# Kernel tuning notes

Measured on AMD Instinct MI355X. Metric: run time of the kernel, lower is better.

## Reference

```python
import jax, jax.numpy as jnp
import numpy as np

B, L, D, Z = 256, 120, 192, 512
H = 2 * Z  # LSTM hidden size


def _lstm_cell(x, h, c, Wih, Whh, bih, bhh):
    # torch LSTMCell gate order: i, f, g, o
    gates = x @ Wih.T + h @ Whh.T + bih + bhh
    i, f, g, o = jnp.split(gates, 4, axis=-1)
    c = jax.nn.sigmoid(f) * c + jax.nn.sigmoid(i) * jnp.tanh(g)
    h = jax.nn.sigmoid(o) * jnp.tanh(c)
    return h, c


def setup_inputs() -> dict:
    key = jax.random.key(0)
    ks = iter(jax.random.split(key, 64))
    def nrm(*shape):
        return jax.random.normal(next(ks), shape, jnp.float32) * 0.02
    inp = {}
    inp["x"] = jax.random.normal(next(ks), (B, L, D), jnp.float32)
    inp["x_lengths"] = jax.random.randint(next(ks), (B,), 1, L + 1)
    # encoder params
    inp["ln_w"] = jnp.ones((L, D), jnp.float32)
    inp["ln_b"] = jnp.zeros((L, D), jnp.float32)
    inp["enc_w"], inp["enc_b"] = nrm(Z, D), nrm(Z)
    for d in ("f", "b"):
        inp["Wih_" + d] = nrm(4 * H, Z)
        inp["Whh_" + d] = nrm(4 * H, H)
        inp["bih_" + d] = nrm(4 * H)
        inp["bhh_" + d] = nrm(4 * H)
    inp["mu1_w"], inp["mu1_b"] = nrm(H, 2 * H), nrm(H)
    inp["mu2_w"], inp["mu2_b"] = nrm(Z, H), nrm(Z)
    inp["lv1_w"], inp["lv1_b"] = nrm(H, 2 * H), nrm(H)
    inp["lv2_w"], inp["lv2_b"] = nrm(Z, H), nrm(Z)
    # decoder params
    inp["dz_w"], inp["dz_b"] = nrm(Z, Z), nrm(Z)
    inp["p1_w"], inp["p1_b"] = nrm(Z, Z), nrm(Z)
    inp["p2_w"], inp["p2_b"] = nrm(D, Z), nrm(D)
    inp["dWih"] = nrm(4 * H, Z + D)
    inp["dWhh"] = nrm(4 * H, H)
    inp["dbih"] = nrm(4 * H)
    inp["dbhh"] = nrm(4 * H)
    inp["l1_w"], inp["l1_b"] = nrm(Z, H), nrm(Z)
    inp["l2_w"], inp["l2_b"] = nrm(D, Z), nrm(D)
    return inp


def _forward(x, x_lengths, ln_w, ln_b, enc_w, enc_b,
             Wih_f, Whh_f, bih_f, bhh_f, Wih_b, Whh_b, bih_b, bhh_b,
             mu1_w, mu1_b, mu2_w, mu2_b, lv1_w, lv1_b, lv2_w, lv2_b,
             dz_w, dz_b, p1_w, p1_b, p2_w, p2_b,
             dWih, dWhh, dbih, dbhh, l1_w, l1_b, l2_w, l2_b):
    relu = jax.nn.relu
    # LayerNorm with normalized_shape=[L, D]: normalize jointly over last two dims
    m = x.mean(axis=(1, 2), keepdims=True)
    v = x.var(axis=(1, 2), keepdims=True)
    xn = (x - m) / jnp.sqrt(v + 1e-5) * ln_w + ln_b
    xe = relu(xn @ enc_w.T + enc_b)          # [B, L, Z]
    xs = xe.transpose(1, 0, 2)               # [L, B, Z]
    ts = jnp.arange(L)

    def make_step(Wih, Whh, bih, bhh):
        def step(carry, inp_t):
            h, c = carry
            xt, t = inp_t
            nh, nc = _lstm_cell(xt, h, c, Wih, Whh, bih, bhh)
            act = (t < x_lengths)[:, None]   # packed-sequence mask
            h = jnp.where(act, nh, h)
            c = jnp.where(act, nc, c)
            return (h, c), jnp.where(act, h, 0.0)  # padded outputs are zero
        return step

    h0 = jnp.zeros((B, H), x.dtype)
    _, out_f = jax.lax.scan(make_step(Wih_f, Whh_f, bih_f, bhh_f), (h0, h0), (xs, ts))
    # backward direction: scan reversed; carry stays zero until first valid step
    _, out_b = jax.lax.scan(make_step(Wih_b, Whh_b, bih_b, bhh_b), (h0, h0), (xs, ts), reverse=True)
    out = jnp.concatenate([out_f, out_b], axis=-1)          # [L, B, 2H]
    pooled = out.sum(axis=0) / x_lengths[:, None].astype(x.dtype)
    mu = relu(pooled @ mu1_w.T + mu1_b) @ mu2_w.T + mu2_b
    log_var = relu(pooled @ lv1_w.T + lv1_b) @ lv2_w.T + lv2_b
    eps = jax.random.normal(jax.random.key(42), mu.shape, mu.dtype)
    z = eps * jnp.exp(0.5 * log_var) + mu
    # decoder with per-step feedback
    xz = relu(z @ dz_w.T + dz_b)
    pose0 = relu(xz @ p1_w.T + p1_b) @ p2_w.T + p2_b

    def dec_step(carry, _):
        h, c, pose = carry
        inp_t = jnp.concatenate([xz, pose], axis=1)
        h, c = _lstm_cell(inp_t, h, c, dWih, dWhh, dbih, dbhh)
        pose = relu(h @ l1_w.T + l1_b) @ l2_w.T + l2_b  # residual=False
        return (h, c, pose), pose

    _, dec = jax.lax.scan(dec_step, (h0, h0, pose0), None, length=L)
    return x, dec.transpose(1, 0, 2), x_lengths, mu, log_var, z


def reference(x, x_lengths, ln_w, ln_b, enc_w, enc_b,
              Wih_f, Whh_f, bih_f, bhh_f, Wih_b, Whh_b, bih_b, bhh_b,
              mu1_w, mu1_b, mu2_w, mu2_b, lv1_w, lv1_b, lv2_w, lv2_b,
              dz_w, dz_b, p1_w, p1_b, p2_w, p2_b,
              dWih, dWhh, dbih, dbhh, l1_w, l1_b, l2_w, l2_b):
    return _forward(x, x_lengths, ln_w, ln_b, enc_w, enc_b,
                    Wih_f, Whh_f, bih_f, bhh_f, Wih_b, Whh_b, bih_b, bhh_b,
                    mu1_w, mu1_b, mu2_w, mu2_b, lv1_w, lv1_b, lv2_w, lv2_b,
                    dz_w, dz_b, p1_w, p1_b, p2_w, p2_b,
                    dWih, dWhh, dbih, dbhh, l1_w, l1_b, l2_w, l2_b)
```

## Files before the change

### kernel.cpp

```cpp
#include <hip/hip_runtime.h>

typedef __bf16 bf16_t;
typedef __bf16 bf16x8 __attribute__((ext_vector_type(8)));
typedef __bf16 bf16x4 __attribute__((ext_vector_type(4)));
typedef float  f32x4  __attribute__((ext_vector_type(4)));

#define DEV __device__ __forceinline__

constexpr int Bn = 256;
constexpr int Ln = 120;
constexpr int Dn = 192;
constexpr int Zn = 512;
constexpr int Hn = 1024;
constexpr int KE = Zn + Hn;
constexpr int KD = Zn + Dn + Hn;
constexpr int CATD = Zn + Dn;
constexpr int NBLK = 256;

DEV f32x4 mfma16(bf16x8 a, bf16x8 b, f32x4 c) {
  return __builtin_amdgcn_mfma_f32_16x16x32_bf16(a, b, c, 0, 0, 0);
}
DEV bf16x8 ldb8(const bf16_t* p) { return *reinterpret_cast<const bf16x8*>(p); }
DEV float sigf(float x) { return 1.f / (1.f + expf(-x)); }
DEV unsigned short b2u(bf16_t v) { union { bf16_t b; unsigned short u; } x; x.b = v; return x.u; }

DEV void ld4i(const bf16_t* p0, const bf16_t* p1, const bf16_t* p2, const bf16_t* p3,
              bf16x8& o0, bf16x8& o1, bf16x8& o2, bf16x8& o3) {
  asm volatile(
      "global_load_dwordx4 %0, %4, off sc0 sc1\n\t"
      "global_load_dwordx4 %1, %5, off sc0 sc1\n\t"
      "global_load_dwordx4 %2, %6, off sc0 sc1\n\t"
      "global_load_dwordx4 %3, %7, off sc0 sc1"
      : "=&v"(o0), "=&v"(o1), "=&v"(o2), "=&v"(o3)
      : "v"(p0), "v"(p1), "v"(p2), "v"(p3)
      : "memory");
}
DEV void ld8i(const bf16_t* p0, const bf16_t* p1, const bf16_t* p2, const bf16_t* p3,
              const bf16_t* p4, const bf16_t* p5, const bf16_t* p6, const bf16_t* p7,
              bf16x8& o0, bf16x8& o1, bf16x8& o2, bf16x8& o3,
              bf16x8& o4, bf16x8& o5, bf16x8& o6, bf16x8& o7) {
  asm volatile(
      "global_load_dwordx4 %0, %8, off sc0 sc1\n\t"
      "global_load_dwordx4 %1, %9, off sc0 sc1\n\t"
      "global_load_dwordx4 %2, %10, off sc0 sc1\n\t"
      "global_load_dwordx4 %3, %11, off sc0 sc1\n\t"
      "global_load_dwordx4 %4, %12, off sc0 sc1\n\t"
      "global_load_dwordx4 %5, %13, off sc0 sc1\n\t"
      "global_load_dwordx4 %6, %14, off sc0 sc1\n\t"
      "global_load_dwordx4 %7, %15, off sc0 sc1"
      : "=&v"(o0), "=&v"(o1), "=&v"(o2), "=&v"(o3),
        "=&v"(o4), "=&v"(o5), "=&v"(o6), "=&v"(o7)
      : "v"(p0), "v"(p1), "v"(p2), "v"(p3), "v"(p4), "v"(p5), "v"(p6), "v"(p7)
      : "memory");
}
DEV void vwait0() {
  asm volatile("s_waitcnt vmcnt(0)" ::: "memory");
  __builtin_amdgcn_sched_barrier(0);
}

DEV void st16c(bf16_t* p, bf16x8 v) {
  asm volatile("global_store_dwordx4 %0, %1, off sc0 sc1" :: "v"(p), "v"(v) : "memory");
}
DEV void st8c(bf16_t* p, bf16x4 v) {
  asm volatile("global_store_dwordx2 %0, %1, off sc0 sc1" :: "v"(p), "v"(v) : "memory");
}
DEV void st2c(bf16_t* p, unsigned short v) {
  asm volatile("global_store_short %0, %1, off sc0 sc1" :: "v"(p), "v"(v) : "memory");
}

DEV void gbar(unsigned* bar, unsigned epoch, int bid) {
  asm volatile("s_waitcnt vmcnt(0)" ::: "memory");
  __syncthreads();
  if (threadIdx.x == 0) {
    int g = bid & 7;
    unsigned a = __hip_atomic_fetch_add(bar + g * 16, 1u, __ATOMIC_RELAXED,
                                        __HIP_MEMORY_SCOPE_AGENT);
    if (a == epoch * 32u - 1u) {
      unsigned b = __hip_atomic_fetch_add(bar + 128, 1u, __ATOMIC_RELAXED,
                                          __HIP_MEMORY_SCOPE_AGENT);
      if (b == epoch * 8u - 1u)
        __hip_atomic_store(bar + 192, epoch, __ATOMIC_RELAXED, __HIP_MEMORY_SCOPE_AGENT);
    }
    while (__hip_atomic_load(bar + 192, __ATOMIC_RELAXED, __HIP_MEMORY_SCOPE_AGENT) < epoch)
      __builtin_amdgcn_s_sleep(2);
  }
  __syncthreads();
}

__global__ void k_cast_all(
    const float* __restrict__ s0, const float* __restrict__ s1,
    const float* __restrict__ s2, const float* __restrict__ s3,
    const float* __restrict__ s4, const float* __restrict__ s5,
    const float* __restrict__ s6, const float* __restrict__ s7,
    const float* __restrict__ s8, const float* __restrict__ s9,
    bf16_t* __restrict__ d0, bf16_t* __restrict__ d1,
    bf16_t* __restrict__ d2, bf16_t* __restrict__ d3,
    bf16_t* __restrict__ d4, bf16_t* __restrict__ d5,
    bf16_t* __restrict__ d6, bf16_t* __restrict__ d7,
    bf16_t* __restrict__ d8, bf16_t* __restrict__ d9) {
  const long TOT = 1646592;
  for (long gidx = blockIdx.x * blockDim.x + threadIdx.x; gidx < TOT;
       gidx += (long)gridDim.x * blockDim.x) {
    const float* s; bf16_t* d; long r = gidx;
    if      (r < 24576)                      { s = s0; d = d0; }
    else if ((r -= 24576)   < 524288)        { s = s1; d = d1; }
    else if ((r -= 524288)  < 524288)        { s = s2; d = d2; }
    else if ((r -= 524288)  < 131072)        { s = s3; d = d3; }
    else if ((r -= 131072)  < 131072)        { s = s4; d = d4; }
    else if ((r -= 131072)  < 65536)         { s = s5; d = d5; }
    else if ((r -= 65536)   < 65536)         { s = s6; d = d6; }
    else if ((r -= 65536)   < 24576)         { s = s7; d = d7; }
    else if ((r -= 24576)   < 131072)        { s = s8; d = d8; }
    else    { r -= 131072;                     s = s9; d = d9; }
    float4 v = reinterpret_cast<const float4*>(s)[r];
    bf16x4 o;
    o[0] = (bf16_t)v.x; o[1] = (bf16_t)v.y; o[2] = (bf16_t)v.z; o[3] = (bf16_t)v.w;
    *reinterpret_cast<bf16x4*>(d + 4 * r) = o;
  }
}

__global__ void k_layernorm(const float* __restrict__ x, const float* __restrict__ w,
                            const float* __restrict__ bsh, float* __restrict__ out0,
                            bf16_t* __restrict__ xn) {
  const int n = Ln * Dn;
  int b = blockIdx.x;
  const float* xb = x + (long)b * n;
  float s = 0.f, s2 = 0.f;
  for (int i = threadIdx.x; i < n; i += 256) { float v = xb[i]; s += v; s2 += v * v; }
  for (int off = 32; off; off >>= 1) { s += __shfl_down(s, off); s2 += __shfl_down(s2, off); }
  __shared__ float sh[8];
  int wave = threadIdx.x >> 6, lane = threadIdx.x & 63;
  if (lane == 0) { sh[wave] = s; sh[4 + wave] = s2; }
  __syncthreads();
  if (threadIdx.x == 0) {
    float S = sh[0] + sh[1] + sh[2] + sh[3];
    float S2 = sh[4] + sh[5] + sh[6] + sh[7];
    float m = S / n;
    float var = fmaxf(S2 / n - m * m, 0.f);
    sh[0] = m; sh[1] = rsqrtf(var + 1e-5f);
  }
  __syncthreads();
  float m = sh[0], inv = sh[1];
  for (int i = threadIdx.x; i < n; i += 256) {
    float v = xb[i];
    out0[(long)b * n + i] = v;
    xn[(long)b * n + i] = (bf16_t)((v - m) * inv * w[i] + bsh[i]);
  }
}

template <int ACT, bool XSPERM>
__global__ __launch_bounds__(256) void k_gemm(
    const bf16_t* __restrict__ A, int lda,
    const bf16_t* __restrict__ W, int ldw,
    const float* __restrict__ bias,
    float* __restrict__ outF, long ldoF,
    bf16_t* __restrict__ outB, int ldoB,
    int K) {
  int lane = threadIdx.x & 63, wave = threadIdx.x >> 6;
  int l15 = lane & 15, q = lane >> 4;
  int m0 = blockIdx.x * 64 + (wave >> 1) * 32;
  int n0 = blockIdx.y * 64 + (wave & 1) * 32;
  f32x4 acc00 = {}, acc01 = {}, acc10 = {}, acc11 = {};
  const bf16_t* Ap = A + (long)(m0 + l15) * lda + q * 8;
  const bf16_t* Wp = W + (long)(n0 + l15) * ldw + q * 8;
  long a16 = (long)16 * lda, w16 = (long)16 * ldw;
  for (int k0 = 0; k0 < K; k0 += 32) {
    bf16x8 a0 = ldb8(Ap + k0);
    bf16x8 a1 = ldb8(Ap + a16 + k0);
    bf16x8 b0 = ldb8(Wp + k0);
    bf16x8 b1 = ldb8(Wp + w16 + k0);
    acc00 = mfma16(a0, b0, acc00);
    acc01 = mfma16(a0, b1, acc01);
    acc10 = mfma16(a1, b0, acc10);
    acc11 = mfma16(a1, b1, acc11);
  }
#pragma unroll
  for (int mi = 0; mi < 2; ++mi)
#pragma unroll
    for (int ni = 0; ni < 2; ++ni) {
      f32x4 acc = (mi == 0) ? (ni == 0 ? acc00 : acc01) : (ni == 0 ? acc10 : acc11);
#pragma unroll
      for (int r = 0; r < 4; ++r) {
        int m = m0 + mi * 16 + q * 4 + r;
        int nn = n0 + ni * 16 + l15;
        float v = acc[r] + bias[nn];
        if (ACT == 1) v = fmaxf(v, 0.f);
        if (outF) outF[(long)m * ldoF + nn] = v;
        if (outB) {
          long row = XSPERM ? ((long)(m % Ln) * Bn + m / Ln) : m;
          outB[row * (long)ldoB + nn] = (bf16_t)v;
        }
      }
    }
}

constexpr int ENC_CH = KE / 32;
constexpr int ENC_SMEM_W = 2 * ENC_CH * 64 * 16;
constexpr int ENC_SMEM_G = 4 * 64 * 33 * 4;
constexpr int ENC_SMEM = ENC_SMEM_W + ENC_SMEM_G + 128;

__global__ __launch_bounds__(256, 1) void k_enc_persist(
    const bf16_t* __restrict__ xs,
    const float* __restrict__ WihF, const float* __restrict__ WhhF,
    const float* __restrict__ bihF, const float* __restrict__ bhhF,
    const float* __restrict__ WihB, const float* __restrict__ WhhB,
    const float* __restrict__ bihB, const float* __restrict__ bhhB,
    const int* __restrict__ lens,
    bf16_t* __restrict__ hf0, bf16_t* __restrict__ hf1,
    bf16_t* __restrict__ hb0, bf16_t* __restrict__ hb1,
    bf16_t* __restrict__ pooledb, float* __restrict__ out_len,
    unsigned* bar) {
  extern __shared__ char smem[];
  bf16x8* Wl = (bf16x8*)smem;
  float* Gbuf = (float*)(smem + ENC_SMEM_W);
  float* bias_l = (float*)(smem + ENC_SMEM_W + ENC_SMEM_G);

  int bid = blockIdx.x;
  int dir = bid >> 7;
  int j0 = (bid & 127) * 8;
  const float* Wih = dir ? WihB : WihF;
  const float* Whh = dir ? WhhB : WhhF;
  const float* bih = dir ? bihB : bihF;
  const float* bhh = dir ? bhhB : bhhF;
  bf16_t* h0 = dir ? hb0 : hf0;
  bf16_t* h1 = dir ? hb1 : hf1;

  int tid = threadIdx.x;
  for (int f = tid; f < 2 * ENC_CH * 64; f += 256) {
    int ni = f / (ENC_CH * 64);
    int rem = f - ni * (ENC_CH * 64);
    int c = rem >> 6, sub = rem & 63;
    int sl = sub & 15, sq = sub >> 4;
    int r = ni * 16 + sl;
    int grow = (r >> 3) * Hn + j0 + (r & 7);
    int k = c * 32 + sq * 8;
    const float* src = (k < Zn) ? (Wih + (long)grow * Zn + k)
                                : (Whh + (long)grow * Hn + (k - Zn));
    bf16x8 v;
#pragma unroll
    for (int e = 0; e < 8; ++e) v[e] = (bf16_t)src[e];
    Wl[f] = v;
  }
  if (tid < 32) {
    int grow = (tid >> 3) * Hn + j0 + (tid & 7);
    bias_l[tid] = bih[grow] + bhh[grow];
  }
  if (bid == 0) out_len[tid] = (float)lens[tid];
  __syncthreads();

  int wave = tid >> 6, lane = tid & 63;
  int l15 = lane & 15, q = lane >> 4;
  int mrow = wave * 64 + l15;
  int m = wave * 64 + lane;
  int mylen = lens[m];
  float c_reg[8] = {}, h_reg[8] = {}, pool_reg[8] = {};
  float* Gw = Gbuf + wave * (64 * 33);
  const bf16x8* Wl0 = Wl;
  const bf16x8* Wl1 = Wl + ENC_CH * 64;
  const long h16 = (long)16 * Hn;

#define ENC_HISS(A, c) do { long hk_ = (long)(c) * 32 - Zn;                               \
    ld8i(hrow + hk_,            hrow + h16 + hk_,                                         \
         hrow + 2 * h16 + hk_,  hrow + 3 * h16 + hk_,                                     \
         hrow + hk_ + 32,       hrow + h16 + hk_ + 32,                                    \
         hrow + 2 * h16 + hk_ + 32, hrow + 3 * h16 + hk_ + 32,                            \
         A[0], A[1], A[2], A[3], A[4], A[5], A[6], A[7]); } while (0)
#define ENC_HCONS(A, c) do {                                                              \
    { bf16x8 b0 = Wl0[(c) * 64 + lane], b1 = Wl1[(c) * 64 + lane];                        \
      acc[0][0] = mfma16(A[0], b0, acc[0][0]); acc[0][1] = mfma16(A[0], b1, acc[0][1]);   \
      acc[1][0] = mfma16(A[1], b0, acc[1][0]); acc[1][1] = mfma16(A[1], b1, acc[1][1]);   \
      acc[2][0] = mfma16(A[2], b0, acc[2][0]); acc[2][1] = mfma16(A[2], b1, acc[2][1]);   \
      acc[3][0] = mfma16(A[3], b0, acc[3][0]); acc[3][1] = mfma16(A[3], b1, acc[3][1]); } \
    { bf16x8 b0 = Wl0[((c) + 1) * 64 + lane], b1 = Wl1[((c) + 1) * 64 + lane];            \
      acc[0][0] = mfma16(A[4], b0, acc[0][0]); acc[0][1] = mfma16(A[4], b1, acc[0][1]);   \
      acc[1][0] = mfma16(A[5], b0, acc[1][0]); acc[1][1] = mfma16(A[5], b1, acc[1][1]);   \
      acc[2][0] = mfma16(A[6], b0, acc[2][0]); acc[2][1] = mfma16(A[6], b1, acc[2][1]);   \
      acc[3][0] = mfma16(A[7], b0, acc[3][0]); acc[3][1] = mfma16(A[7], b1, acc[3][1]); } \
  } while (0)
#define ENC_STEP(Acur, Anext, c) vwait0(); ENC_HISS(Anext, (c) + 2); ENC_HCONS(Acur, c);

  for (int t = 0; t < Ln; ++t) {
    int tt = dir ? (Ln - 1 - t) : t;
    const bf16_t* xt = xs + (long)tt * Bn * Zn;
    const bf16_t* hprev = (t & 1) ? h1 : h0;
    bf16_t* hcur = (t & 1) ? h0 : h1;

    f32x4 acc[4][2] = {};
    const bf16_t* xrow = xt + (long)mrow * Zn + q * 8;
    const bf16_t* hrow = hprev + (long)mrow * Hn + q * 8;

    bf16x8 HA[8], HB[8];
    ENC_HISS(HA, 16);
    for (int c = 0; c < Zn / 32; ++c) {
      bf16x8 b0 = Wl0[c * 64 + lane];
      bf16x8 b1 = Wl1[c * 64 + lane];
#pragma unroll
      for (int mi = 0; mi < 4; ++mi) {
        bf16x8 a = ldb8(xrow + (long)mi * 16 * Zn + c * 32);
        acc[mi][0] = mfma16(a, b0, acc[mi][0]);
        acc[mi][1] = mfma16(a, b1, acc[mi][1]);
      }
    }
    ENC_STEP(HA, HB, 16) ENC_STEP(HB, HA, 18) ENC_STEP(HA, HB, 20) ENC_STEP(HB, HA, 22)
    ENC_STEP(HA, HB, 24) ENC_STEP(HB, HA, 26) ENC_STEP(HA, HB, 28) ENC_STEP(HB, HA, 30)
    ENC_STEP(HA, HB, 32) ENC_STEP(HB, HA, 34) ENC_STEP(HA, HB, 36) ENC_STEP(HB, HA, 38)
    ENC_STEP(HA, HB, 40) ENC_STEP(HB, HA, 42) ENC_STEP(HA, HB, 44)
    vwait0(); ENC_HCONS(HB, 46);

#pragma unroll
    for (int mi = 0; mi < 4; ++mi)
#pragma unroll
      for (int ni = 0; ni < 2; ++ni)
#pragma unroll
        for (int r = 0; r < 4; ++r)
          Gw[(mi * 16 + q * 4 + r) * 33 + ni * 16 + l15] = acc[mi][ni][r];
    __syncthreads();
    bool act = tt < mylen;
    const float* Gr = Gw + lane * 33;
    bf16x8 hpack;
#pragma unroll
    for (int jj = 0; jj < 8; ++jj) {
      float Gi = Gr[jj] + bias_l[jj];
      float Gf = Gr[8 + jj] + bias_l[8 + jj];
      float Gg = Gr[16 + jj] + bias_l[16 + jj];
      float Go = Gr[24 + jj] + bias_l[24 + jj];
      float cn = sigf(Gf) * c_reg[jj] + sigf(Gi) * tanhf(Gg);
      float hn = sigf(Go) * tanhf(cn);
      if (act) { c_reg[jj] = cn; h_reg[jj] = hn; pool_reg[jj] += hn; }
      hpack[jj] = (bf16_t)h_reg[jj];
    }
    st16c(hcur + (long)m * Hn + j0, hpack);
    if (t != Ln - 1) gbar(bar, (unsigned)(t + 1), bid);
  }
#undef ENC_STEP
#undef ENC_HCONS
#undef ENC_HISS
  bf16x8 pp;
#pragma unroll
  for (int jj = 0; jj < 8; ++jj) pp[jj] = (bf16_t)(pool_reg[jj] / (float)mylen);
  *(bf16x8*)(pooledb + (long)m * (2 * Hn) + dir * Hn + j0) = pp;
}

constexpr int DEC_CH = KD / 32;
constexpr int DEC_SMEM_W = 2 * DEC_CH * 64 * 16;
constexpr int DEC_SMEM_G = 4 * 32 * 33 * 4;
constexpr int DEC_SMEM = DEC_SMEM_W + DEC_SMEM_G + 128;

__global__ __launch_bounds__(256, 1) void k_dec_persist(
    bf16_t* __restrict__ inp,
    const float* __restrict__ dWih, const float* __restrict__ dWhh,
    const float* __restrict__ dbih, const float* __restrict__ dbhh,
    bf16_t* __restrict__ h_in0, bf16_t* __restrict__ h_in1,
    const bf16_t* __restrict__ l1w, const float* __restrict__ l1bias,
    const bf16_t* __restrict__ l2w, const float* __restrict__ l2bias,
    bf16_t* __restrict__ t1,
    float* __restrict__ out_dec,
    unsigned* bar) {
  extern __shared__ char smem[];
  bf16x8* Wl = (bf16x8*)smem;
  float* Gbuf = (float*)(smem + DEC_SMEM_W);
  float* bias_l = (float*)(smem + DEC_SMEM_W + DEC_SMEM_G);

  int bid = blockIdx.x;
  int mbase = (bid >> 7) * 128;
  int j0 = (bid & 127) * 8;
  int tid = threadIdx.x;

  for (int f = tid; f < 2 * DEC_CH * 64; f += 256) {
    int ni = f / (DEC_CH * 64);
    int rem = f - ni * (DEC_CH * 64);
    int c = rem >> 6, sub = rem & 63;
    int sl = sub & 15, sq = sub >> 4;
    int r = ni * 16 + sl;
    int grow = (r >> 3) * Hn + j0 + (r & 7);
    int k = c * 32 + sq * 8;
    const float* src = (k < CATD) ? (dWih + (long)grow * CATD + k)
                                  : (dWhh + (long)grow * Hn + (k - CATD));
    bf16x8 v;
#pragma unroll
    for (int e = 0; e < 8; ++e) v[e] = (bf16_t)src[e];
    Wl[f] = v;
  }
  if (tid < 32) {
    int grow = (tid >> 3) * Hn + j0 + (tid & 7);
    bias_l[tid] = dbih[grow] + dbhh[grow];
  }
  __syncthreads();

  int wave = tid >> 6, lane = tid & 63;
  int l15 = lane & 15, q = lane >> 4;
  int mrow = mbase + wave * 32 + l15;
  int mpt = mbase + wave * 32 + (lane >> 1);
  int jh = (lane & 1) * 4;
  float c_reg[4] = {};
  float* Gw = Gbuf + wave * (32 * 33);
  int gw = bid * 4 + wave;
  const bf16x8* Wl0 = Wl;
  const bf16x8* Wl1 = Wl + DEC_CH * 64;
  const long i16 = (long)16 * CATD;
  const long h16d = (long)16 * Hn;

#define DEC_HISS(A, c) do { long hk_ = (long)(c) * 32 - CATD;                             \
    ld8i(hrow + hk_,        hrow + h16d + hk_,                                            \
         hrow + hk_ + 32,   hrow + h16d + hk_ + 32,                                       \
         hrow + hk_ + 64,   hrow + h16d + hk_ + 64,                                       \
         hrow + hk_ + 96,   hrow + h16d + hk_ + 96,                                       \
         A[0], A[1], A[2], A[3], A[4], A[5], A[6], A[7]); } while (0)
#define DEC_HCONS(A, c) do {                                                              \
    { bf16x8 b0 = Wl0[(c) * 64 + lane], b1 = Wl1[(c) * 64 + lane];                        \
      acc[0][0] = mfma16(A[0], b0, acc[0][0]); acc[0][1] = mfma16(A[0], b1, acc[0][1]);   \
      acc[1][0] = mfma16(A[1], b0, acc[1][0]); acc[1][1] = mfma16(A[1], b1, acc[1][1]); } \
    { bf16x8 b0 = Wl0[((c) + 1) * 64 + lane], b1 = Wl1[((c) + 1) * 64 + lane];            \
      acc[0][0] = mfma16(A[2], b0, acc[0][0]); acc[0][1] = mfma16(A[2], b1, acc[0][1]);   \
      acc[1][0] = mfma16(A[3], b0, acc[1][0]); acc[1][1] = mfma16(A[3], b1, acc[1][1]); } \
    { bf16x8 b0 = Wl0[((c) + 2) * 64 + lane], b1 = Wl1[((c) + 2) * 64 + lane];            \
      acc[0][0] = mfma16(A[4], b0, acc[0][0]); acc[0][1] = mfma16(A[4], b1, acc[0][1]);   \
      acc[1][0] = mfma16(A[5], b0, acc[1][0]); acc[1][1] = mfma16(A[5], b1, acc[1][1]); } \
    { bf16x8 b0 = Wl0[((c) + 3) * 64 + lane], b1 = Wl1[((c) + 3) * 64 + lane];            \
      acc[0][0] = mfma16(A[6], b0, acc[0][0]); acc[0][1] = mfma16(A[6], b1, acc[0][1]);   \
      acc[1][0] = mfma16(A[7], b0, acc[1][0]); acc[1][1] = mfma16(A[7], b1, acc[1][1]); } \
  } while (0)

  for (int t = 0; t < Ln; ++t) {
    const bf16_t* hprev = (t & 1) ? h_in1 : h_in0;
    bf16_t* hcur = (t & 1) ? h_in0 : h_in1;

    f32x4 acc[2][2] = {};
    const bf16_t* irow = inp + (long)mrow * CATD + q * 8;
    const bf16_t* hrow = hprev + (long)mrow * Hn + q * 8;

    bf16x8 P0, P1, P2, P3, P4, P5, P6, P7, P8, P9, P10, P11;
    ld8i(irow + 16 * 32, irow + i16 + 16 * 32, irow + 17 * 32, irow + i16 + 17 * 32,
         irow + 18 * 32, irow + i16 + 18 * 32, irow + 19 * 32, irow + i16 + 19 * 32,
         P0, P1, P2, P3, P4, P5, P6, P7);
    ld4i(irow + 20 * 32, irow + i16 + 20 * 32, irow + 21 * 32, irow + i16 + 21 * 32,
         P8, P9, P10, P11);
    bf16x8 HA[8], HB[8];
    DEC_HISS(HA, 22);

    for (int c = 0; c < Zn / 32; ++c) {
      bf16x8 b0 = Wl0[c * 64 + lane];
      bf16x8 b1 = Wl1[c * 64 + lane];
#pragma unroll
      for (int mi = 0; mi < 2; ++mi) {
        bf16x8 a = ldb8(irow + (long)mi * 16 * CATD + c * 32);
        acc[mi][0] = mfma16(a, b0, acc[mi][0]);
        acc[mi][1] = mfma16(a, b1, acc[mi][1]);
      }
    }
    vwait0();
    DEC_HISS(HB, 26);
    { bf16x8 b0 = Wl0[16 * 64 + lane], b1 = Wl1[16 * 64 + lane];
      acc[0][0] = mfma16(P0, b0, acc[0][0]); acc[0][1] = mfma16(P0, b1, acc[0][1]);
      acc[1][0] = mfma16(P1, b0, acc[1][0]); acc[1][1] = mfma16(P1, b1, acc[1][1]); }
    { bf16x8 b0 = Wl0[17 * 64 + lane], b1 = Wl1[17 * 64 + lane];
      acc[0][0] = mfma16(P2, b0, acc[0][0]); acc[0][1] = mfma16(P2, b1, acc[0][1]);
      acc[1][0] = mfma16(P3, b0, acc[1][0]); acc[1][1] = mfma16(P3, b1, acc[1][1]); }
    { bf16x8 b0 = Wl0[18 * 64 + lane], b1 = Wl1[18 * 64 + lane];
      acc[0][0] = mfma16(P4, b0, acc[0][0]); acc[0][1] = mfma16(P4, b1, acc[0][1]);
      acc[1][0] = mfma16(P5, b0, acc[1][0]); acc[1][1] = mfma16(P5, b1, acc[1][1]); }
    { bf16x8 b0 = Wl0[19 * 64 + lane], b1 = Wl1[19 * 64 + lane];
      acc[0][0] = mfma16(P6, b0, acc[0][0]); acc[0][1] = mfma16(P6, b1, acc[0][1]);
      acc[1][0] = mfma16(P7, b0, acc[1][0]); acc[1][1] = mfma16(P7, b1, acc[1][1]); }
    { bf16x8 b0 = Wl0[20 * 64 + lane], b1 = Wl1[20 * 64 + lane];
      acc[0][0] = mfma16(P8, b0, acc[0][0]); acc[0][1] = mfma16(P8, b1, acc[0][1]);
      acc[1][0] = mfma16(P9, b0, acc[1][0]); acc[1][1] = mfma16(P9, b1, acc[1][1]); }
    { bf16x8 b0 = Wl0[21 * 64 + lane], b1 = Wl1[21 * 64 + lane];
      acc[0][0] = mfma16(P10, b0, acc[0][0]); acc[0][1] = mfma16(P10, b1, acc[0][1]);
      acc[1][0] = mfma16(P11, b0, acc[1][0]); acc[1][1] = mfma16(P11, b1, acc[1][1]); }
    DEC_HCONS(HA, 22);
    vwait0(); DEC_HISS(HA, 30); DEC_HCONS(HB, 26);
    vwait0(); DEC_HISS(HB, 34); DEC_HCONS(HA, 30);
    vwait0(); DEC_HISS(HA, 38); DEC_HCONS(HB, 34);
    vwait0(); DEC_HISS(HB, 42); DEC_HCONS(HA, 38);
    vwait0(); DEC_HISS(HA, 46); DEC_HCONS(HB, 42);
    vwait0(); DEC_HISS(HB, 50); DEC_HCONS(HA, 46);
    vwait0(); DEC_HCONS(HB, 50);

#pragma unroll
    for (int mi = 0; mi < 2; ++mi)
#pragma unroll
      for (int ni = 0; ni < 2; ++ni)
#pragma unroll
        for (int r = 0; r < 4; ++r)
          Gw[(mi * 16 + q * 4 + r) * 33 + ni * 16 + l15] = acc[mi][ni][r];
    __syncthreads();
    {
      const float* Gr = Gw + (lane >> 1) * 33 + jh;
      bf16x4 hp;
#pragma unroll
      for (int p = 0; p < 4; ++p) {
        float Gi = Gr[p] + bias_l[jh + p];
        float Gf = Gr[8 + p] + bias_l[8 + jh + p];
        float Gg = Gr[16 + p] + bias_l[16 + jh + p];
        float Go = Gr[24 + p] + bias_l[24 + jh + p];
        float cn = sigf(Gf) * c_reg[p] + sigf(Gi) * tanhf(Gg);
        c_reg[p] = cn;
        hp[p] = (bf16_t)(sigf(Go) * tanhf(cn));
      }
      st8c(hcur + (long)mpt * Hn + j0 + jh, hp);
    }
    gbar(bar, (unsigned)(3 * t + 1), bid);

    if (gw < 512) {
      int mt = gw >> 5, nt = gw & 31;
      f32x4 a1 = {};
      const bf16_t* ha = hcur + (long)(mt * 16 + l15) * Hn + q * 8;
      const bf16_t* wb = l1w + (long)(nt * 16 + l15) * Hn + q * 8;
      bf16x8 QA[8], QB[8];
#define P2_ISS(A, c0) ld8i(ha + ((c0) + 0) * 32, ha + ((c0) + 1) * 32,                    \
                           ha + ((c0) + 2) * 32, ha + ((c0) + 3) * 32,                    \
                           ha + ((c0) + 4) * 32, ha + ((c0) + 5) * 32,                    \
                           ha + ((c0) + 6) * 32, ha + ((c0) + 7) * 32,                    \
                           A[0], A[1], A[2], A[3], A[4], A[5], A[6], A[7])
      P2_ISS(QA, 0);
      vwait0(); P2_ISS(QB, 8);
#pragma unroll
      for (int k = 0; k < 8; ++k) a1 = mfma16(QA[k], ldb8(wb + k * 32), a1);
      vwait0(); P2_ISS(QA, 16);
#pragma unroll
      for (int k = 0; k < 8; ++k) a1 = mfma16(QB[k], ldb8(wb + (8 + k) * 32), a1);
      vwait0(); P2_ISS(QB, 24);
#pragma unroll
      for (int k = 0; k < 8; ++k) a1 = mfma16(QA[k], ldb8(wb + (16 + k) * 32), a1);
      vwait0();
#pragma unroll
      for (int k = 0; k < 8; ++k) a1 = mfma16(QB[k], ldb8(wb + (24 + k) * 32), a1);
#undef P2_ISS
      int n = nt * 16 + l15;
      float bb = l1bias[n];
#pragma unroll
      for (int r = 0; r < 4; ++r) {
        float v = fmaxf(a1[r] + bb, 0.f);
        st2c(t1 + (long)(mt * 16 + q * 4 + r) * Zn + n, b2u((bf16_t)v));
      }
    }
    gbar(bar, (unsigned)(3 * t + 2), bid);

    if (gw < 192) {
      int mt = gw / 12, nt = gw - mt * 12;
      f32x4 a2 = {};
      const bf16_t* ta = t1 + (long)(mt * 16 + l15) * Zn + q * 8;
      const bf16_t* wb = l2w + (long)(nt * 16 + l15) * Zn + q * 8;
      bf16x8 QA[8], QB[8];
      ld8i(ta + 0 * 32, ta + 1 * 32, ta + 2 * 32, ta + 3 * 32,
           ta + 4 * 32, ta + 5 * 32, ta + 6 * 32, ta + 7 * 32,
           QA[0], QA[1], QA[2], QA[3], QA[4], QA[5], QA[6], QA[7]);
      vwait0();
      ld8i(ta + 8 * 32, ta + 9 * 32, ta + 10 * 32, ta + 11 * 32,
           ta + 12 * 32, ta + 13 * 32, ta + 14 * 32, ta + 15 * 32,
           QB[0], QB[1], QB[2], QB[3], QB[4], QB[5], QB[6], QB[7]);
#pragma unroll
      for (int k = 0; k < 8; ++k) a2 = mfma16(QA[k], ldb8(wb + k * 32), a2);
      vwait0();
#pragma unroll
      for (int k = 0; k < 8; ++k) a2 = mfma16(QB[k], ldb8(wb + (8 + k) * 32), a2);
      int n = nt * 16 + l15;
      float bb = l2bias[n];
#pragma unroll
      for (int r = 0; r < 4; ++r) {
        int mm = mt * 16 + q * 4 + r;
        float v = a2[r] + bb;
        out_dec[(long)mm * (Ln * Dn) + (long)t * Dn + n] = v;
        st2c(inp + (long)mm * CATD + Zn + n, b2u((bf16_t)v));
      }
    }
    if (t != Ln - 1) gbar(bar, (unsigned)(3 * t + 3), bid);
  }
#undef DEC_HCONS
#undef DEC_HISS
}

DEV unsigned rotl32(unsigned v, int s) { return (v << s) | (v >> (32 - s)); }

#define TF_R4(r0, r1, r2, r3)                       \
  x0 += x1; x1 = rotl32(x1, r0); x1 ^= x0;          \
  x0 += x1; x1 = rotl32(x1, r1); x1 ^= x0;          \
  x0 += x1; x1 = rotl32(x1, r2); x1 ^= x0;          \
  x0 += x1; x1 = rotl32(x1, r3); x1 ^= x0;

DEV float erfinv_xla(float x) {
  float w = -log1pf(-x * x);
  float p;
  if (w < 5.f) {
    w -= 2.5f;
    p = 2.81022636e-08f;
    p = fmaf(p, w, 3.43273939e-07f);
    p = fmaf(p, w, -3.5233877e-06f);
    p = fmaf(p, w, -4.39150654e-06f);
    p = fmaf(p, w, 0.00021858087f);
    p = fmaf(p, w, -0.00125372503f);
    p = fmaf(p, w, -0.00417768164f);
    p = fmaf(p, w, 0.246640727f);
    p = fmaf(p, w, 1.50140941f);
  } else {
    w = sqrtf(w) - 3.f;
    p = -0.000200214257f;
    p = fmaf(p, w, 0.000100950558f);
    p = fmaf(p, w, 0.00134934322f);
    p = fmaf(p, w, -0.00367342844f);
    p = fmaf(p, w, 0.00573950773f);
    p = fmaf(p, w, -0.0076224613f);
    p = fmaf(p, w, 0.00943887047f);
    p = fmaf(p, w, 1.00167406f);
    p = fmaf(p, w, 2.83297682f);
  }
  return p * x;
}

__global__ void k_z(const float* __restrict__ mu, const float* __restrict__ lv,
                    float* __restrict__ zf, bf16_t* __restrict__ zb) {
  int i = blockIdx.x * blockDim.x + threadIdx.x;
  const unsigned ks0 = 0u, ks1 = 42u, ks2 = 0x1BD11BDAu ^ ks0 ^ ks1;
  unsigned x0 = 0u + ks0;
  unsigned x1 = (unsigned)i + ks1;
  TF_R4(13, 15, 26, 6);  x0 += ks1; x1 += ks2 + 1u;
  TF_R4(17, 29, 16, 24); x0 += ks2; x1 += ks0 + 2u;
  TF_R4(13, 15, 26, 6);  x0 += ks0; x1 += ks1 + 3u;
  TF_R4(17, 29, 16, 24); x0 += ks1; x1 += ks2 + 4u;
  TF_R4(13, 15, 26, 6);  x0 += ks2; x1 += ks0 + 5u;
  unsigned bits = x0 ^ x1;
  float f = __uint_as_float((bits >> 9) | 0x3F800000u) - 1.0f;
  float u = f * 2.0f + (-0.99999994f);
  u = fmaxf(u, -0.99999994f);
  float e = 1.41421356f * erfinv_xla(u);
  float zv = e * expf(0.5f * lv[i]) + mu[i];
  zf[i] = zv;
  zb[i] = (bf16_t)zv;
}

extern "C" void kernel_launch(void* const* d_in, const int* in_sizes, int n_in,
                              void* d_out, int out_size, void* d_ws, size_t ws_size,
                              hipStream_t stream) {
  const float* x     = (const float*)d_in[0];
  const int*   lens  = (const int*)d_in[1];
  const float* ln_w  = (const float*)d_in[2];
  const float* ln_b  = (const float*)d_in[3];
  const float* enc_w = (const float*)d_in[4];
  const float* enc_b = (const float*)d_in[5];
  const float* Wih_f = (const float*)d_in[6];
  const float* Whh_f = (const float*)d_in[7];
  const float* bih_f = (const float*)d_in[8];
  const float* bhh_f = (const float*)d_in[9];
  const float* Wih_b = (const float*)d_in[10];
  const float* Whh_b = (const float*)d_in[11];
  const float* bih_b = (const float*)d_in[12];
  const float* bhh_b = (const float*)d_in[13];
  const float* mu1_w = (const float*)d_in[14];
  const float* mu1_b = (const float*)d_in[15];
  const float* mu2_w = (const float*)d_in[16];
  const float* mu2_b = (const float*)d_in[17];
  const float* lv1_w = (const float*)d_in[18];
  const float* lv1_b = (const float*)d_in[19];
  const float* lv2_w = (const float*)d_in[20];
  const float* lv2_b = (const float*)d_in[21];
  const float* dz_w  = (const float*)d_in[22];
  const float* dz_b  = (const float*)d_in[23];
  const float* p1_w  = (const float*)d_in[24];
  const float* p1_b  = (const float*)d_in[25];
  const float* p2_w  = (const float*)d_in[26];
  const float* p2_b  = (const float*)d_in[27];
  const float* dWih  = (const float*)d_in[28];
  const float* dWhh  = (const float*)d_in[29];
  const float* dbih  = (const float*)d_in[30];
  const float* dbhh  = (const float*)d_in[31];
  const float* l1_w  = (const float*)d_in[32];
  const float* l1_b  = (const float*)d_in[33];
  const float* l2_w  = (const float*)d_in[34];
  const float* l2_b  = (const float*)d_in[35];

  float* out0    = (float*)d_out;
  float* out_dec = out0 + (long)Bn * Ln * Dn;
  float* out_len = out_dec + (long)Bn * Ln * Dn;
  float* out_mu  = out_len + Bn;
  float* out_lv  = out_mu + (long)Bn * Zn;
  float* out_z   = out_lv + (long)Bn * Zn;

  char* wp = (char*)d_ws;
  auto alloc = [&](size_t bytes) -> void* {
    void* r = (void*)wp;
    wp += (bytes + 255) & ~(size_t)255;
    return r;
  };

  bf16_t* xn      = (bf16_t*)alloc((size_t)Bn * Ln * Dn * 2);
  bf16_t* xs      = (bf16_t*)alloc((size_t)Ln * Bn * Zn * 2);
  bf16_t* encw    = (bf16_t*)alloc((size_t)Zn * Dn * 2);
  bf16_t* mu1b    = (bf16_t*)alloc((size_t)Hn * 2 * Hn * 2);
  bf16_t* lv1b    = (bf16_t*)alloc((size_t)Hn * 2 * Hn * 2);
  bf16_t* mu2b    = (bf16_t*)alloc((size_t)Zn * Hn * 2);
  bf16_t* lv2b    = (bf16_t*)alloc((size_t)Zn * Hn * 2);
  bf16_t* dzb     = (bf16_t*)alloc((size_t)Zn * Zn * 2);
  bf16_t* p1b     = (bf16_t*)alloc((size_t)Zn * Zn * 2);
  bf16_t* p2b     = (bf16_t*)alloc((size_t)Dn * Zn * 2);
  bf16_t* l1b     = (bf16_t*)alloc((size_t)Zn * Hn * 2);
  bf16_t* l2b     = (bf16_t*)alloc((size_t)Dn * Zn * 2);
  bf16_t* hf0     = (bf16_t*)alloc((size_t)Bn * Hn * 2);
  bf16_t* hf1     = (bf16_t*)alloc((size_t)Bn * Hn * 2);
  bf16_t* hb0     = (bf16_t*)alloc((size_t)Bn * Hn * 2);
  bf16_t* hb1     = (bf16_t*)alloc((size_t)Bn * Hn * 2);
  bf16_t* hd0     = (bf16_t*)alloc((size_t)Bn * Hn * 2);
  bf16_t* hd1     = (bf16_t*)alloc((size_t)Bn * Hn * 2);
  bf16_t* pooledb = (bf16_t*)alloc((size_t)Bn * 2 * Hn * 2);
  bf16_t* mu_h    = (bf16_t*)alloc((size_t)Bn * Hn * 2);
  bf16_t* lv_h    = (bf16_t*)alloc((size_t)Bn * Hn * 2);
  bf16_t* zb      = (bf16_t*)alloc((size_t)Bn * Zn * 2);
  bf16_t* inp     = (bf16_t*)alloc((size_t)Bn * CATD * 2);
  bf16_t* t1      = (bf16_t*)alloc((size_t)Bn * Zn * 2);
  unsigned* bars  = (unsigned*)alloc(2048);
  unsigned* barE  = bars;
  unsigned* barD  = bars + 256;

  static int s_attr_done = 0;
  if (!s_attr_done) {
    (void)hipFuncSetAttribute((const void*)k_enc_persist,
                              hipFuncAttributeMaxDynamicSharedMemorySize, ENC_SMEM);
    (void)hipFuncSetAttribute((const void*)k_dec_persist,
                              hipFuncAttributeMaxDynamicSharedMemorySize, DEC_SMEM);
    s_attr_done = 1;
  }

  hipMemsetAsync(hf0, 0, (size_t)Bn * Hn * 2, stream);
  hipMemsetAsync(hb0, 0, (size_t)Bn * Hn * 2, stream);
  hipMemsetAsync(hd0, 0, (size_t)Bn * Hn * 2, stream);
  hipMemsetAsync(bars, 0, 2048, stream);

  k_cast_all<<<2048, 256, 0, stream>>>(enc_w, mu1_w, lv1_w, mu2_w, lv2_w,
                                       dz_w, p1_w, p2_w, l1_w, l2_w,
                                       encw, mu1b, lv1b, mu2b, lv2b,
                                       dzb, p1b, p2b, l1b, l2b);

  k_layernorm<<<256, 256, 0, stream>>>(x, ln_w, ln_b, out0, xn);

  k_gemm<1, true><<<dim3(480, 8), 256, 0, stream>>>(xn, Dn, encw, Dn, enc_b,
                                                    nullptr, 0, xs, Zn, Dn);

  {
    void* ea[] = {&xs, &Wih_f, &Whh_f, &bih_f, &bhh_f,
                  &Wih_b, &Whh_b, &bih_b, &bhh_b, &lens,
                  &hf0, &hf1, &hb0, &hb1, &pooledb, &out_len, &barE};
    hipLaunchCooperativeKernel((const void*)k_enc_persist, dim3(256), dim3(256),
                               ea, (unsigned)ENC_SMEM, stream);
  }

  k_gemm<1, false><<<dim3(4, 16), 256, 0, stream>>>(pooledb, 2 * Hn, mu1b, 2 * Hn, mu1_b,
                                                    nullptr, 0, mu_h, Hn, 2 * Hn);
  k_gemm<1, false><<<dim3(4, 16), 256, 0, stream>>>(pooledb, 2 * Hn, lv1b, 2 * Hn, lv1_b,
                                                    nullptr, 0, lv_h, Hn, 2 * Hn);
  k_gemm<0, false><<<dim3(4, 8), 256, 0, stream>>>(mu_h, Hn, mu2b, Hn, mu2_b,
                                                   out_mu, Zn, nullptr, 0, Hn);
  k_gemm<0, false><<<dim3(4, 8), 256, 0, stream>>>(lv_h, Hn, lv2b, Hn, lv2_b,
                                                   out_lv, Zn, nullptr, 0, Hn);

  k_z<<<512, 256, 0, stream>>>(out_mu, out_lv, out_z, zb);

  k_gemm<1, false><<<dim3(4, 8), 256, 0, stream>>>(zb, Zn, dzb, Zn, dz_b,
                                                   nullptr, 0, inp, CATD, Zn);
  k_gemm<1, false><<<dim3(4, 8), 256, 0, stream>>>(inp, CATD, p1b, Zn, p1_b,
                                                   nullptr, 0, t1, Zn, Zn);
  k_gemm<0, false><<<dim3(4, 3), 256, 0, stream>>>(t1, Zn, p2b, Zn, p2_b,
                                                   nullptr, 0, inp + Zn, CATD, Zn);

  {
    void* da[] = {&inp, &dWih, &dWhh, &dbih, &dbhh, &hd0, &hd1,
                  &l1b, &l1_b, &l2b, &l2_b, &t1, &out_dec, &barD};
    hipLaunchCooperativeKernel((const void*)k_dec_persist, dim3(256), dim3(256),
                               da, (unsigned)DEC_SMEM, stream);
  }
}
```

Before: 8.026 ms.

## Fuse decoder pose MLP into 16 blocks and drop one grid barrier per step

The two pose projection GEMMs (l1 then l2) move from a 512-wave and a 192-wave distribution, separated by a grid-wide barrier, into 16 blocks. Each block computes a full 16-row slice of t1, keeps it in shared memory and then applies l2 locally. This removes one grid barrier per timestep and the global round trip for t1. In exchange, this phase runs on far fewer CUs and each block reads the whole l1 and l2 weights per step, which may lengthen the critical path.

```diff
diff --git a/kernel.cpp b/kernel.cpp
--- a/kernel.cpp
+++ b/kernel.cpp
@@ -353,7 +353,6 @@
     bf16_t* __restrict__ h_in0, bf16_t* __restrict__ h_in1,
     const bf16_t* __restrict__ l1w, const float* __restrict__ l1bias,
     const bf16_t* __restrict__ l2w, const float* __restrict__ l2bias,
-    bf16_t* __restrict__ t1,
     float* __restrict__ out_dec,
     unsigned* bar) {
   extern __shared__ char smem[];
@@ -394,7 +393,6 @@
   int jh = (lane & 1) * 4;
   float c_reg[4] = {};
   float* Gw = Gbuf + wave * (32 * 33);
-  int gw = bid * 4 + wave;
   const bf16x8* Wl0 = Wl;
   const bf16x8* Wl1 = Wl + DEC_CH * 64;
   const long i16 = (long)16 * CATD;
@@ -500,72 +498,69 @@
       }
       st8c(hcur + (long)mpt * Hn + j0 + jh, hp);
     }
-    gbar(bar, (unsigned)(3 * t + 1), bid);
-
-    if (gw < 512) {
-      int mt = gw >> 5, nt = gw & 31;
-      f32x4 a1 = {};
-      const bf16_t* ha = hcur + (long)(mt * 16 + l15) * Hn + q * 8;
-      const bf16_t* wb = l1w + (long)(nt * 16 + l15) * Hn + q * 8;
+    gbar(bar, (unsigned)(2 * t + 1), bid);
+
+    if (bid < 16) {
+      int r0 = bid * 16;
+      f32x4 accl[8] = {};
+      const bf16_t* ha = hcur + (long)(r0 + l15) * Hn + q * 8;
+      const bf16_t* wb1 = l1w + (long)(wave * 128 + l15) * Hn + q * 8;
       bf16x8 QA[8], QB[8];
 #define P2_ISS(A, c0) ld8i(ha + ((c0) + 0) * 32, ha + ((c0) + 1) * 32,                    \
                            ha + ((c0) + 2) * 32, ha + ((c0) + 3) * 32,                    \
                            ha + ((c0) + 4) * 32, ha + ((c0) + 5) * 32,                    \
                            ha + ((c0) + 6) * 32, ha + ((c0) + 7) * 32,                    \
                            A[0], A[1], A[2], A[3], A[4], A[5], A[6], A[7])
+#define P2_CONS(A, c0) do {                                                               \
+    _Pragma("unroll")                                                                     \
+    for (int k_ = 0; k_ < 8; ++k_) {                                                      \
+      _Pragma("unroll")                                                                   \
+      for (int nti = 0; nti < 8; ++nti)                                                   \
+        accl[nti] = mfma16(A[k_], ldb8(wb1 + (long)nti * 16 * Hn + ((c0) + k_) * 32),     \
+                           accl[nti]);                                                    \
+    } } while (0)
       P2_ISS(QA, 0);
-      vwait0(); P2_ISS(QB, 8);
-#pragma unroll
-      for (int k = 0; k < 8; ++k) a1 = mfma16(QA[k], ldb8(wb + k * 32), a1);
-      vwait0(); P2_ISS(QA, 16);
-#pragma unroll
-      for (int k = 0; k < 8; ++k) a1 = mfma16(QB[k], ldb8(wb + (8 + k) * 32), a1);
-      vwait0(); P2_ISS(QB, 24);
-#pragma unroll
-      for (int k = 0; k < 8; ++k) a1 = mfma16(QA[k], ldb8(wb + (16 + k) * 32), a1);
-      vwait0();
-#pragma unroll
-      for (int k = 0; k < 8; ++k) a1 = mfma16(QB[k], ldb8(wb + (24 + k) * 32), a1);
+      vwait0(); P2_ISS(QB, 8);  P2_CONS(QA, 0);
+      vwait0(); P2_ISS(QA, 16); P2_CONS(QB, 8);
+      vwait0(); P2_ISS(QB, 24); P2_CONS(QA, 16);
+      vwait0();                 P2_CONS(QB, 24);
+#undef P2_CONS
 #undef P2_ISS
-      int n = nt * 16 + l15;
-      float bb = l1bias[n];
-#pragma unroll
-      for (int r = 0; r < 4; ++r) {
-        float v = fmaxf(a1[r] + bb, 0.f);
-        st2c(t1 + (long)(mt * 16 + q * 4 + r) * Zn + n, b2u((bf16_t)v));
+      bf16_t* t1l = (bf16_t*)Gbuf;
+#pragma unroll
+      for (int nti = 0; nti < 8; ++nti) {
+        int n = wave * 128 + nti * 16 + l15;
+        float bb = l1bias[n];
+#pragma unroll
+        for (int r = 0; r < 4; ++r)
+          t1l[(q * 4 + r) * 520 + n] = (bf16_t)fmaxf(accl[nti][r] + bb, 0.f);
+      }
+      __syncthreads();
+      f32x4 acc2[3] = {};
+      const bf16_t* ta = t1l + l15 * 520 + q * 8;
+      const bf16_t* wb2 = l2w + (long)(wave * 48 + l15) * Zn + q * 8;
+      for (int c = 0; c < Zn / 32; ++c) {
+        bf16x8 a = *reinterpret_cast<const bf16x8*>(ta + c * 32);
+#pragma unroll
+        for (int i = 0; i < 3; ++i) {
+          bf16x8 b = ldb8(wb2 + (long)i * 16 * Zn + c * 32);
+          acc2[i] = mfma16(a, b, acc2[i]);
+        }
+      }
+#pragma unroll
+      for (int i = 0; i < 3; ++i) {
+        int n = wave * 48 + i * 16 + l15;
+        float bb = l2bias[n];
+#pragma unroll
+        for (int r = 0; r < 4; ++r) {
+          int mm = r0 + q * 4 + r;
+          float v = acc2[i][r] + bb;
+          out_dec[(long)mm * (Ln * Dn) + (long)t * Dn + n] = v;
+          st2c(inp + (long)mm * CATD + Zn + n, b2u((bf16_t)v));
+        }
       }
     }
-    gbar(bar, (unsigned)(3 * t + 2), bid);
-
-    if (gw < 192) {
-      int mt = gw / 12, nt = gw - mt * 12;
-      f32x4 a2 = {};
-      const bf16_t* ta = t1 + (long)(mt * 16 + l15) * Zn + q * 8;
-      const bf16_t* wb = l2w + (long)(nt * 16 + l15) * Zn + q * 8;
-      bf16x8 QA[8], QB[8];
-      ld8i(ta + 0 * 32, ta + 1 * 32, ta + 2 * 32, ta + 3 * 32,
-           ta + 4 * 32, ta + 5 * 32, ta + 6 * 32, ta + 7 * 32,
-           QA[0], QA[1], QA[2], QA[3], QA[4], QA[5], QA[6], QA[7]);
-      vwait0();
-      ld8i(ta + 8 * 32, ta + 9 * 32, ta + 10 * 32, ta + 11 * 32,
-           ta + 12 * 32, ta + 13 * 32, ta + 14 * 32, ta + 15 * 32,
-           QB[0], QB[1], QB[2], QB[3], QB[4], QB[5], QB[6], QB[7]);
-#pragma unroll
-      for (int k = 0; k < 8; ++k) a2 = mfma16(QA[k], ldb8(wb + k * 32), a2);
-      vwait0();
-#pragma unroll
-      for (int k = 0; k < 8; ++k) a2 = mfma16(QB[k], ldb8(wb + (8 + k) * 32), a2);
-      int n = nt * 16 + l15;
-      float bb = l2bias[n];
-#pragma unroll
-      for (int r = 0; r < 4; ++r) {
-        int mm = mt * 16 + q * 4 + r;
-        float v = a2[r] + bb;
-        out_dec[(long)mm * (Ln * Dn) + (long)t * Dn + n] = v;
-        st2c(inp + (long)mm * CATD + Zn + n, b2u((bf16_t)v));
-      }
-    }
-    if (t != Ln - 1) gbar(bar, (unsigned)(3 * t + 3), bid);
+    if (t != Ln - 1) gbar(bar, (unsigned)(2 * t + 2), bid);
   }
 #undef DEC_HCONS
 #undef DEC_HISS
@@ -763,7 +758,7 @@
 
   {
     void* da[] = {&inp, &dWih, &dWhh, &dbih, &dbhh, &hd0, &hd1,
-                  &l1b, &l1_b, &l2b, &l2_b, &t1, &out_dec, &barD};
+                  &l1b, &l1_b, &l2b, &l2_b, &out_dec, &barD};
     hipLaunchCooperativeKernel((const void*)k_dec_persist, dim3(256), dim3(256),
                                da, (unsigned)DEC_SMEM, stream);
   }
```

Measured after the change: 12.58 ms. +56.7%, slower.
